# Kernel tuning notes

Hardware: AMD Instinct MI355X
Metric: run time of the kernel (lower is better)

The kernel has to match this reference:

```python
import jax, jax.numpy as jnp
import numpy as np

N_USERS = 100000
N_ITEMS = 200000
N_NODES = N_USERS + N_ITEMS
LATENT_DIM = 64
N_LAYERS = 3
NNZ = 6400000


def setup_inputs() -> dict:
    key = jax.random.key(0)
    k1, k2, k3, k4, k5 = jax.random.split(key, 5)
    user_emb = 0.1 * jax.random.normal(k1, (N_USERS, LATENT_DIM), dtype=jnp.float32)
    item_emb = 0.1 * jax.random.normal(k2, (N_ITEMS, LATENT_DIM), dtype=jnp.float32)
    rows = jax.random.randint(k3, (NNZ,), 0, N_NODES, dtype=jnp.int32)
    cols = jax.random.randint(k4, (NNZ,), 0, N_NODES, dtype=jnp.int32)
    # normalized-adjacency-like positive values
    vals = jax.random.uniform(k5, (NNZ,), dtype=jnp.float32) * 0.05
    return {"user_emb": user_emb, "item_emb": item_emb,
            "rows": rows, "cols": cols, "vals": vals}


def _spmm(rows, cols, vals, x):
    # y[r] += vals[e] * x[cols[e]]  for each edge e with rows[e]==r
    gathered = vals[:, None] * x[cols]          # [nnz, D]
    return jax.ops.segment_sum(gathered, rows, num_segments=N_NODES)


def reference(user_emb, item_emb, rows, cols, vals):
    # LightGCN.computer(): multi-hop propagation + layer mean pooling
    all_emb = jnp.concatenate([user_emb, item_emb], axis=0)   # [N, D]
    acc = all_emb
    for _ in range(N_LAYERS):
        all_emb = _spmm(rows, cols, vals, all_emb)
        acc = acc + all_emb
    light_out = acc / (N_LAYERS + 1)
    users = light_out[:N_USERS]
    items = light_out[N_USERS:]
    return users, items
```

## Files before the change

kernel.cpp:

```cpp
#include <hip/hip_runtime.h>
#include <hip/hip_bf16.h>

#define N_USERS 100000
#define N_ITEMS 200000
#define N_NODES 300000
#define DIM 64

#define TOT_ELEMS ((size_t)N_NODES * DIM)
#define TOT_F4    (TOT_ELEMS / 4)
#define USER_F4   (((size_t)N_USERS * DIM) / 4)

#define BROWS 512
#define NBUCKET ((N_NODES + BROWS - 1) / BROWS)
#define EPT 32
#define EDGES_PER_BLOCK (EPT * 256)

__device__ __forceinline__ float bf2f(unsigned short u) {
    return __uint_as_float((unsigned int)u << 16);
}
__device__ __forceinline__ unsigned short f2bf(float f) {
    __hip_bfloat16 h = __float2bfloat16(f);
    return *reinterpret_cast<unsigned short*>(&h);
}

__global__ void init_kernel(const float4* __restrict__ user,
                            const float4* __restrict__ item,
                            ushort4* __restrict__ xh) {
    size_t i = (size_t)blockIdx.x * blockDim.x + threadIdx.x;
    if (i >= TOT_F4) return;
    float4 v = (i < USER_F4) ? user[i] : item[i - USER_F4];
    ushort4 h;
    h.x = f2bf(v.x); h.y = f2bf(v.y); h.z = f2bf(v.z); h.w = f2bf(v.w);
    xh[i] = h;
}

__global__ void zero_buckets_kernel(int* __restrict__ bucket_count) {
    int i = blockIdx.x * blockDim.x + threadIdx.x;
    if (i < NBUCKET) bucket_count[i] = 0;
}

__global__ void bucket_hist_kernel(const int* __restrict__ rows,
                                   int* __restrict__ bucket_count, int nnz) {
    __shared__ int h[NBUCKET];
    int t = threadIdx.x;
    size_t base = (size_t)blockIdx.x * EDGES_PER_BLOCK;
    for (int i = t; i < NBUCKET; i += 256) h[i] = 0;
    __syncthreads();
    #pragma unroll 4
    for (int k = 0; k < EPT; ++k) {
        size_t e = base + (size_t)k * 256 + t;
        if (e < (size_t)nnz) atomicAdd(&h[rows[e] >> 9], 1);
    }
    __syncthreads();
    for (int i = t; i < NBUCKET; i += 256) {
        int c = h[i];
        if (c) atomicAdd(&bucket_count[i], c);
    }
}

__global__ void bucket_scan_kernel(const int* __restrict__ bucket_count,
                                   int* __restrict__ bucket_base,
                                   int* __restrict__ bucket_cursor, int nnz) {
    __shared__ int s[1024];
    int t = threadIdx.x;
    int orig = (t < NBUCKET) ? bucket_count[t] : 0;
    s[t] = orig;
    __syncthreads();
    for (int off = 1; off < 1024; off <<= 1) {
        int v = (t >= off) ? s[t - off] : 0;
        __syncthreads();
        s[t] += v;
        __syncthreads();
    }
    if (t < NBUCKET) {
        int excl = s[t] - orig;
        bucket_base[t]   = excl;
        bucket_cursor[t] = excl;
    }
    if (t == 0) bucket_base[NBUCKET] = nnz;
}

__global__ void binA_kernel(const int* __restrict__ rows,
                            const int* __restrict__ cols,
                            const float* __restrict__ vals,
                            int* __restrict__ bucket_cursor,
                            int2* __restrict__ binned,
                            int nnz) {
    __shared__ int h[NBUCKET];
    int t = threadIdx.x;
    size_t base = (size_t)blockIdx.x * EDGES_PER_BLOCK;
    for (int i = t; i < NBUCKET; i += 256) h[i] = 0;
    __syncthreads();
    #pragma unroll 4
    for (int k = 0; k < EPT; ++k) {
        size_t e = base + (size_t)k * 256 + t;
        if (e < (size_t)nnz) atomicAdd(&h[rows[e] >> 9], 1);
    }
    __syncthreads();
    for (int i = t; i < NBUCKET; i += 256) {
        int c = h[i];
        h[i] = (c > 0) ? atomicAdd(&bucket_cursor[i], c) : 0;
    }
    __syncthreads();
    #pragma unroll 4
    for (int k = 0; k < EPT; ++k) {
        size_t e = base + (size_t)k * 256 + t;
        if (e < (size_t)nnz) {
            int r = rows[e];
            int pos = atomicAdd(&h[r >> 9], 1);
            binned[pos] = make_int2(((r & (BROWS - 1)) << 19) | cols[e],
                                    __float_as_int(vals[e]));
        }
    }
}

__global__ void binB_kernel(const int* __restrict__ bucket_base,
                            const int2* __restrict__ binned,
                            int2* __restrict__ sorted,
                            int* __restrict__ row_ptr,
                            int nnz) {
    __shared__ int cnt[BROWS];
    __shared__ int cur[BROWS];
    __shared__ int s[256];
    int b = blockIdx.x, t = threadIdx.x;
    int beg = bucket_base[b];
    int end = bucket_base[b + 1];
    int row0 = b * BROWS;
    for (int i = t; i < BROWS; i += 256) cnt[i] = 0;
    __syncthreads();
    for (int idx = beg + t; idx < end; idx += 256) {
        int lr = ((unsigned)binned[idx].x) >> 19;
        atomicAdd(&cnt[lr], 1);
    }
    __syncthreads();
    int c0 = cnt[2 * t], c1 = cnt[2 * t + 1];
    int local = c0 + c1;
    s[t] = local;
    __syncthreads();
    for (int off = 1; off < 256; off <<= 1) {
        int v = (t >= off) ? s[t - off] : 0;
        __syncthreads();
        s[t] += v;
        __syncthreads();
    }
    int excl = beg + s[t] - local;
    int r0 = row0 + 2 * t;
    if (r0 < N_NODES)     row_ptr[r0]     = excl;
    if (r0 + 1 < N_NODES) row_ptr[r0 + 1] = excl + c0;
    cur[2 * t]     = excl;
    cur[2 * t + 1] = excl + c0;
    __syncthreads();
    for (int idx = beg + t; idx < end; idx += 256) {
        int2 e = binned[idx];
        int lr  = ((unsigned)e.x) >> 19;
        int col = e.x & 0x7FFFF;
        int pos = atomicAdd(&cur[lr], 1);
        sorted[pos] = make_int2(col, e.y);
    }
    if (b == 0 && t == 0) row_ptr[N_NODES] = nnz;
}

__device__ __forceinline__ float row_accum(int beg, int end, int d,
                                           const int2* __restrict__ sorted,
                                           const unsigned short* __restrict__ srch) {
    float acc = 0.f;
    for (int base = beg; base < end; base += 64) {
        int rem = end - base;
        int cnt = rem > 64 ? 64 : rem;
        int c_l = 0;
        int v_i = 0;
        if (base + d < end) {
            int2 e = sorted[base + d];
            c_l = e.x;
            v_i = e.y;
        }
        int j = 0;
        for (; j + 8 <= cnt; j += 8) {
            int c0 = __builtin_amdgcn_readlane(c_l, j + 0);
            int c1 = __builtin_amdgcn_readlane(c_l, j + 1);
            int c2 = __builtin_amdgcn_readlane(c_l, j + 2);
            int c3 = __builtin_amdgcn_readlane(c_l, j + 3);
            int c4 = __builtin_amdgcn_readlane(c_l, j + 4);
            int c5 = __builtin_amdgcn_readlane(c_l, j + 5);
            int c6 = __builtin_amdgcn_readlane(c_l, j + 6);
            int c7 = __builtin_amdgcn_readlane(c_l, j + 7);
            float s0 = bf2f(srch[(size_t)c0 * DIM + d]);
            float s1 = bf2f(srch[(size_t)c1 * DIM + d]);
            float s2 = bf2f(srch[(size_t)c2 * DIM + d]);
            float s3 = bf2f(srch[(size_t)c3 * DIM + d]);
            float s4 = bf2f(srch[(size_t)c4 * DIM + d]);
            float s5 = bf2f(srch[(size_t)c5 * DIM + d]);
            float s6 = bf2f(srch[(size_t)c6 * DIM + d]);
            float s7 = bf2f(srch[(size_t)c7 * DIM + d]);
            float v0 = __uint_as_float(__builtin_amdgcn_readlane(v_i, j + 0));
            float v1 = __uint_as_float(__builtin_amdgcn_readlane(v_i, j + 1));
            float v2 = __uint_as_float(__builtin_amdgcn_readlane(v_i, j + 2));
            float v3 = __uint_as_float(__builtin_amdgcn_readlane(v_i, j + 3));
            float v4 = __uint_as_float(__builtin_amdgcn_readlane(v_i, j + 4));
            float v5 = __uint_as_float(__builtin_amdgcn_readlane(v_i, j + 5));
            float v6 = __uint_as_float(__builtin_amdgcn_readlane(v_i, j + 6));
            float v7 = __uint_as_float(__builtin_amdgcn_readlane(v_i, j + 7));
            acc += v0 * s0; acc += v1 * s1; acc += v2 * s2; acc += v3 * s3;
            acc += v4 * s4; acc += v5 * s5; acc += v6 * s6; acc += v7 * s7;
        }
        for (; j + 4 <= cnt; j += 4) {
            int c0 = __builtin_amdgcn_readlane(c_l, j + 0);
            int c1 = __builtin_amdgcn_readlane(c_l, j + 1);
            int c2 = __builtin_amdgcn_readlane(c_l, j + 2);
            int c3 = __builtin_amdgcn_readlane(c_l, j + 3);
            float s0 = bf2f(srch[(size_t)c0 * DIM + d]);
            float s1 = bf2f(srch[(size_t)c1 * DIM + d]);
            float s2 = bf2f(srch[(size_t)c2 * DIM + d]);
            float s3 = bf2f(srch[(size_t)c3 * DIM + d]);
            float v0 = __uint_as_float(__builtin_amdgcn_readlane(v_i, j + 0));
            float v1 = __uint_as_float(__builtin_amdgcn_readlane(v_i, j + 1));
            float v2 = __uint_as_float(__builtin_amdgcn_readlane(v_i, j + 2));
            float v3 = __uint_as_float(__builtin_amdgcn_readlane(v_i, j + 3));
            acc += v0 * s0; acc += v1 * s1; acc += v2 * s2; acc += v3 * s3;
        }
        for (; j < cnt; ++j) {
            int c = __builtin_amdgcn_readlane(c_l, j);
            float v = __uint_as_float(__builtin_amdgcn_readlane(v_i, j));
            acc += v * bf2f(srch[(size_t)c * DIM + d]);
        }
    }
    return acc;
}

__global__ void spmm_row_kernel(const int* __restrict__ row_ptr,
                                const int2* __restrict__ sorted,
                                const unsigned short* __restrict__ srch,
                                unsigned short* __restrict__ dsth) {
    int t = blockIdx.x * blockDim.x + threadIdx.x;
    int r = t >> 6;
    int d = t & 63;
    if (r >= N_NODES) return;
    float acc = row_accum(row_ptr[r], row_ptr[r + 1], d, sorted, srch);
    dsth[(size_t)r * DIM + d] = f2bf(acc);
}

__global__ void spmm_final_kernel(const int* __restrict__ row_ptr,
                                  const int2* __restrict__ sorted,
                                  const unsigned short* __restrict__ y2h,
                                  const unsigned short* __restrict__ y1h,
                                  const float* __restrict__ user,
                                  const float* __restrict__ item,
                                  float* __restrict__ out) {
    int t = blockIdx.x * blockDim.x + threadIdx.x;
    int r = t >> 6;
    int d = t & 63;
    if (r >= N_NODES) return;
    float acc = row_accum(row_ptr[r], row_ptr[r + 1], d, sorted, y2h);
    size_t idx = (size_t)r * DIM + d;
    float base = (r < N_USERS) ? user[idx]
                               : item[idx - (size_t)N_USERS * DIM];
    out[idx] = 0.25f * (base + bf2f(y1h[idx]) + bf2f(y2h[idx]) + acc);
}

extern "C" void kernel_launch(void* const* d_in, const int* in_sizes, int n_in,
                              void* d_out, int out_size, void* d_ws, size_t ws_size,
                              hipStream_t stream) {
    const float* user = (const float*)d_in[0];
    const float* item = (const float*)d_in[1];
    const int*   rows = (const int*)d_in[2];
    const int*   cols = (const int*)d_in[3];
    const float* vals = (const float*)d_in[4];
    int nnz = in_sizes[2];

    float* out = (float*)d_out;

    char* p = (char*)d_ws;
    unsigned short* xh  = (unsigned short*)p; p += TOT_ELEMS * 2;
    unsigned short* y1h = (unsigned short*)p; p += TOT_ELEMS * 2;
    unsigned short* y2h = (unsigned short*)p; p += TOT_ELEMS * 2;
    int2* binned = (int2*)p; p += (size_t)nnz * sizeof(int2);
    int2* sorted = (int2*)p; p += (size_t)nnz * sizeof(int2);
    int* row_ptr       = (int*)p; p += (size_t)(N_NODES + 1) * 4;
    int* bucket_count  = (int*)p; p += (size_t)NBUCKET * 4;
    int* bucket_base   = (int*)p; p += (size_t)(NBUCKET + 1) * 4;
    int* bucket_cursor = (int*)p; p += (size_t)NBUCKET * 4;

    const int BLK = 256;
    int grid_elem = (int)((TOT_F4 + BLK - 1) / BLK);
    int grid_binA = (nnz + EDGES_PER_BLOCK - 1) / EDGES_PER_BLOCK;
    int grid_rows = (N_NODES * 64 + BLK - 1) / BLK;

    init_kernel<<<grid_elem, BLK, 0, stream>>>(
        (const float4*)user, (const float4*)item, (ushort4*)xh);

    zero_buckets_kernel<<<(NBUCKET + BLK - 1) / BLK, BLK, 0, stream>>>(bucket_count);
    bucket_hist_kernel<<<grid_binA, BLK, 0, stream>>>(rows, bucket_count, nnz);
    bucket_scan_kernel<<<1, 1024, 0, stream>>>(bucket_count, bucket_base, bucket_cursor, nnz);

    binA_kernel<<<grid_binA, BLK, 0, stream>>>(rows, cols, vals, bucket_cursor, binned, nnz);
    binB_kernel<<<NBUCKET, BLK, 0, stream>>>(bucket_base, binned, sorted, row_ptr, nnz);

    spmm_row_kernel<<<grid_rows, BLK, 0, stream>>>(row_ptr, sorted, xh,  y1h);
    spmm_row_kernel<<<grid_rows, BLK, 0, stream>>>(row_ptr, sorted, y1h, y2h);
    spmm_final_kernel<<<grid_rows, BLK, 0, stream>>>(row_ptr, sorted, y2h, y1h,
                                                     user, item, out);
}
```

Measured before the change: 916.0 us.

## Split wavefront into two edge halves gathering packed bf16 pairs per lane

The row SpMM kernel now has each 32-lane half of a wavefront handle alternate edges. Each lane loads a 32-bit pair of bf16 features and keeps two accumulators, and the halves are combined with a cross-half shuffle at the end. Edge indices are broadcast with ds_bpermute instead of scalar readlane, so each half gets a different edge. The goal is to halve the number of gather load instructions per edge and widen each access. Nontemporal loads and stores are also added to the streaming reads in init, binning and the final combine. The cost is an extra shuffle reduction and LDS-permute traffic per edge.

After: 887.8 us. -3.1%, faster.

```diff
diff --git a/kernel.cpp b/kernel.cpp
--- a/kernel.cpp
+++ b/kernel.cpp
@@ -15,6 +15,8 @@
 #define EPT 32
 #define EDGES_PER_BLOCK (EPT * 256)
 
+typedef float f4_native __attribute__((ext_vector_type(4)));
+
 __device__ __forceinline__ float bf2f(unsigned short u) {
     return __uint_as_float((unsigned int)u << 16);
 }
@@ -22,13 +24,21 @@
     __hip_bfloat16 h = __float2bfloat16(f);
     return *reinterpret_cast<unsigned short*>(&h);
 }
-
-__global__ void init_kernel(const float4* __restrict__ user,
-                            const float4* __restrict__ item,
+__device__ __forceinline__ float lo_bf(unsigned int u) {
+    return __uint_as_float(u << 16);
+}
+__device__ __forceinline__ float hi_bf(unsigned int u) {
+    return __uint_as_float(u & 0xFFFF0000u);
+}
+
+__global__ void init_kernel(const float* __restrict__ user,
+                            const float* __restrict__ item,
                             ushort4* __restrict__ xh) {
     size_t i = (size_t)blockIdx.x * blockDim.x + threadIdx.x;
     if (i >= TOT_F4) return;
-    float4 v = (i < USER_F4) ? user[i] : item[i - USER_F4];
+    f4_native v = (i < USER_F4)
+        ? __builtin_nontemporal_load((const f4_native*)user + i)
+        : __builtin_nontemporal_load((const f4_native*)item + (i - USER_F4));
     ushort4 h;
     h.x = f2bf(v.x); h.y = f2bf(v.y); h.z = f2bf(v.z); h.w = f2bf(v.w);
     xh[i] = h;
@@ -108,8 +118,10 @@
         if (e < (size_t)nnz) {
             int r = rows[e];
             int pos = atomicAdd(&h[r >> 9], 1);
-            binned[pos] = make_int2(((r & (BROWS - 1)) << 19) | cols[e],
-                                    __float_as_int(vals[e]));
+            int c   = __builtin_nontemporal_load(cols + e);
+            float v = __builtin_nontemporal_load(vals + e);
+            binned[pos] = make_int2(((r & (BROWS - 1)) << 19) | c,
+                                    __float_as_int(v));
         }
     }
 }
@@ -160,71 +172,92 @@
     if (b == 0 && t == 0) row_ptr[N_NODES] = nnz;
 }
 
-__device__ __forceinline__ float row_accum(int beg, int end, int d,
+__device__ __forceinline__ void row_accum2(int beg, int end, int l,
                                            const int2* __restrict__ sorted,
-                                           const unsigned short* __restrict__ srch) {
-    float acc = 0.f;
+                                           const unsigned short* __restrict__ srch,
+                                           float& r0, float& r1) {
+    const int h4 = (l >> 5) << 2;
+    const unsigned int q = (unsigned)(l & 31);
+    const unsigned int* __restrict__ srcd = (const unsigned int*)srch;
+    float acc0 = 0.f, acc1 = 0.f;
+
     for (int base = beg; base < end; base += 64) {
         int rem = end - base;
         int cnt = rem > 64 ? 64 : rem;
-        int c_l = 0;
-        int v_i = 0;
-        if (base + d < end) {
-            int2 e = sorted[base + d];
-            c_l = e.x;
-            v_i = e.y;
-        }
-        int j = 0;
-        for (; j + 8 <= cnt; j += 8) {
-            int c0 = __builtin_amdgcn_readlane(c_l, j + 0);
-            int c1 = __builtin_amdgcn_readlane(c_l, j + 1);
-            int c2 = __builtin_amdgcn_readlane(c_l, j + 2);
-            int c3 = __builtin_amdgcn_readlane(c_l, j + 3);
-            int c4 = __builtin_amdgcn_readlane(c_l, j + 4);
-            int c5 = __builtin_amdgcn_readlane(c_l, j + 5);
-            int c6 = __builtin_amdgcn_readlane(c_l, j + 6);
-            int c7 = __builtin_amdgcn_readlane(c_l, j + 7);
-            float s0 = bf2f(srch[(size_t)c0 * DIM + d]);
-            float s1 = bf2f(srch[(size_t)c1 * DIM + d]);
-            float s2 = bf2f(srch[(size_t)c2 * DIM + d]);
-            float s3 = bf2f(srch[(size_t)c3 * DIM + d]);
-            float s4 = bf2f(srch[(size_t)c4 * DIM + d]);
-            float s5 = bf2f(srch[(size_t)c5 * DIM + d]);
-            float s6 = bf2f(srch[(size_t)c6 * DIM + d]);
-            float s7 = bf2f(srch[(size_t)c7 * DIM + d]);
-            float v0 = __uint_as_float(__builtin_amdgcn_readlane(v_i, j + 0));
-            float v1 = __uint_as_float(__builtin_amdgcn_readlane(v_i, j + 1));
-            float v2 = __uint_as_float(__builtin_amdgcn_readlane(v_i, j + 2));
-            float v3 = __uint_as_float(__builtin_amdgcn_readlane(v_i, j + 3));
-            float v4 = __uint_as_float(__builtin_amdgcn_readlane(v_i, j + 4));
-            float v5 = __uint_as_float(__builtin_amdgcn_readlane(v_i, j + 5));
-            float v6 = __uint_as_float(__builtin_amdgcn_readlane(v_i, j + 6));
-            float v7 = __uint_as_float(__builtin_amdgcn_readlane(v_i, j + 7));
-            acc += v0 * s0; acc += v1 * s1; acc += v2 * s2; acc += v3 * s3;
-            acc += v4 * s4; acc += v5 * s5; acc += v6 * s6; acc += v7 * s7;
-        }
-        for (; j + 4 <= cnt; j += 4) {
-            int c0 = __builtin_amdgcn_readlane(c_l, j + 0);
-            int c1 = __builtin_amdgcn_readlane(c_l, j + 1);
-            int c2 = __builtin_amdgcn_readlane(c_l, j + 2);
-            int c3 = __builtin_amdgcn_readlane(c_l, j + 3);
-            float s0 = bf2f(srch[(size_t)c0 * DIM + d]);
-            float s1 = bf2f(srch[(size_t)c1 * DIM + d]);
-            float s2 = bf2f(srch[(size_t)c2 * DIM + d]);
-            float s3 = bf2f(srch[(size_t)c3 * DIM + d]);
-            float v0 = __uint_as_float(__builtin_amdgcn_readlane(v_i, j + 0));
-            float v1 = __uint_as_float(__builtin_amdgcn_readlane(v_i, j + 1));
-            float v2 = __uint_as_float(__builtin_amdgcn_readlane(v_i, j + 2));
-            float v3 = __uint_as_float(__builtin_amdgcn_readlane(v_i, j + 3));
-            acc += v0 * s0; acc += v1 * s1; acc += v2 * s2; acc += v3 * s3;
-        }
-        for (; j < cnt; ++j) {
-            int c = __builtin_amdgcn_readlane(c_l, j);
-            float v = __uint_as_float(__builtin_amdgcn_readlane(v_i, j));
-            acc += v * bf2f(srch[(size_t)c * DIM + d]);
-        }
-    }
-    return acc;
+        int c_l = 0, v_l = 0;
+        if (base + l < end) {
+            unsigned long long e = __builtin_nontemporal_load(
+                (const unsigned long long*)sorted + base + l);
+            c_l = (int)(unsigned int)(e & 0xFFFFFFFFull);
+            v_l = (int)(unsigned int)(e >> 32);
+        }
+        int npairs = (cnt + 1) >> 1;
+        int p = 0;
+        for (; p + 8 <= npairs; p += 8) {
+            int i0 = h4 + (p << 3);
+            int c0 = __builtin_amdgcn_ds_bpermute(i0 +  0, c_l);
+            int c1 = __builtin_amdgcn_ds_bpermute(i0 +  8, c_l);
+            int c2 = __builtin_amdgcn_ds_bpermute(i0 + 16, c_l);
+            int c3 = __builtin_amdgcn_ds_bpermute(i0 + 24, c_l);
+            int c4 = __builtin_amdgcn_ds_bpermute(i0 + 32, c_l);
+            int c5 = __builtin_amdgcn_ds_bpermute(i0 + 40, c_l);
+            int c6 = __builtin_amdgcn_ds_bpermute(i0 + 48, c_l);
+            int c7 = __builtin_amdgcn_ds_bpermute(i0 + 56, c_l);
+            unsigned int u0 = srcd[((unsigned int)c0 << 5) | q];
+            unsigned int u1 = srcd[((unsigned int)c1 << 5) | q];
+            unsigned int u2 = srcd[((unsigned int)c2 << 5) | q];
+            unsigned int u3 = srcd[((unsigned int)c3 << 5) | q];
+            unsigned int u4 = srcd[((unsigned int)c4 << 5) | q];
+            unsigned int u5 = srcd[((unsigned int)c5 << 5) | q];
+            unsigned int u6 = srcd[((unsigned int)c6 << 5) | q];
+            unsigned int u7 = srcd[((unsigned int)c7 << 5) | q];
+            float v0 = __int_as_float(__builtin_amdgcn_ds_bpermute(i0 +  0, v_l));
+            float v1 = __int_as_float(__builtin_amdgcn_ds_bpermute(i0 +  8, v_l));
+            float v2 = __int_as_float(__builtin_amdgcn_ds_bpermute(i0 + 16, v_l));
+            float v3 = __int_as_float(__builtin_amdgcn_ds_bpermute(i0 + 24, v_l));
+            float v4 = __int_as_float(__builtin_amdgcn_ds_bpermute(i0 + 32, v_l));
+            float v5 = __int_as_float(__builtin_amdgcn_ds_bpermute(i0 + 40, v_l));
+            float v6 = __int_as_float(__builtin_amdgcn_ds_bpermute(i0 + 48, v_l));
+            float v7 = __int_as_float(__builtin_amdgcn_ds_bpermute(i0 + 56, v_l));
+            acc0 = fmaf(v0, lo_bf(u0), acc0); acc1 = fmaf(v0, hi_bf(u0), acc1);
+            acc0 = fmaf(v1, lo_bf(u1), acc0); acc1 = fmaf(v1, hi_bf(u1), acc1);
+            acc0 = fmaf(v2, lo_bf(u2), acc0); acc1 = fmaf(v2, hi_bf(u2), acc1);
+            acc0 = fmaf(v3, lo_bf(u3), acc0); acc1 = fmaf(v3, hi_bf(u3), acc1);
+            acc0 = fmaf(v4, lo_bf(u4), acc0); acc1 = fmaf(v4, hi_bf(u4), acc1);
+            acc0 = fmaf(v5, lo_bf(u5), acc0); acc1 = fmaf(v5, hi_bf(u5), acc1);
+            acc0 = fmaf(v6, lo_bf(u6), acc0); acc1 = fmaf(v6, hi_bf(u6), acc1);
+            acc0 = fmaf(v7, lo_bf(u7), acc0); acc1 = fmaf(v7, hi_bf(u7), acc1);
+        }
+        for (; p + 4 <= npairs; p += 4) {
+            int i0 = h4 + (p << 3);
+            int c0 = __builtin_amdgcn_ds_bpermute(i0 +  0, c_l);
+            int c1 = __builtin_amdgcn_ds_bpermute(i0 +  8, c_l);
+            int c2 = __builtin_amdgcn_ds_bpermute(i0 + 16, c_l);
+            int c3 = __builtin_amdgcn_ds_bpermute(i0 + 24, c_l);
+            unsigned int u0 = srcd[((unsigned int)c0 << 5) | q];
+            unsigned int u1 = srcd[((unsigned int)c1 << 5) | q];
+            unsigned int u2 = srcd[((unsigned int)c2 << 5) | q];
+            unsigned int u3 = srcd[((unsigned int)c3 << 5) | q];
+            float v0 = __int_as_float(__builtin_amdgcn_ds_bpermute(i0 +  0, v_l));
+            float v1 = __int_as_float(__builtin_amdgcn_ds_bpermute(i0 +  8, v_l));
+            float v2 = __int_as_float(__builtin_amdgcn_ds_bpermute(i0 + 16, v_l));
+            float v3 = __int_as_float(__builtin_amdgcn_ds_bpermute(i0 + 24, v_l));
+            acc0 = fmaf(v0, lo_bf(u0), acc0); acc1 = fmaf(v0, hi_bf(u0), acc1);
+            acc0 = fmaf(v1, lo_bf(u1), acc0); acc1 = fmaf(v1, hi_bf(u1), acc1);
+            acc0 = fmaf(v2, lo_bf(u2), acc0); acc1 = fmaf(v2, hi_bf(u2), acc1);
+            acc0 = fmaf(v3, lo_bf(u3), acc0); acc1 = fmaf(v3, hi_bf(u3), acc1);
+        }
+        for (; p < npairs; ++p) {
+            int i0 = h4 + (p << 3);
+            int c0 = __builtin_amdgcn_ds_bpermute(i0, c_l);
+            unsigned int u0 = srcd[((unsigned int)c0 << 5) | q];
+            float v0 = __int_as_float(__builtin_amdgcn_ds_bpermute(i0, v_l));
+            acc0 = fmaf(v0, lo_bf(u0), acc0);
+            acc1 = fmaf(v0, hi_bf(u0), acc1);
+        }
+    }
+    r0 = acc0 + __shfl_xor(acc0, 32);
+    r1 = acc1 + __shfl_xor(acc1, 32);
 }
 
 __global__ void spmm_row_kernel(const int* __restrict__ row_ptr,
@@ -233,10 +266,14 @@
                                 unsigned short* __restrict__ dsth) {
     int t = blockIdx.x * blockDim.x + threadIdx.x;
     int r = t >> 6;
-    int d = t & 63;
+    int l = t & 63;
     if (r >= N_NODES) return;
-    float acc = row_accum(row_ptr[r], row_ptr[r + 1], d, sorted, srch);
-    dsth[(size_t)r * DIM + d] = f2bf(acc);
+    float r0, r1;
+    row_accum2(row_ptr[r], row_ptr[r + 1], l, sorted, srch, r0, r1);
+    if (l < 32) {
+        unsigned int pack = (unsigned int)f2bf(r0) | ((unsigned int)f2bf(r1) << 16);
+        ((unsigned int*)dsth)[(size_t)r * 32 + l] = pack;
+    }
 }
 
 __global__ void spmm_final_kernel(const int* __restrict__ row_ptr,
@@ -248,13 +285,23 @@
                                   float* __restrict__ out) {
     int t = blockIdx.x * blockDim.x + threadIdx.x;
     int r = t >> 6;
-    int d = t & 63;
+    int l = t & 63;
     if (r >= N_NODES) return;
-    float acc = row_accum(row_ptr[r], row_ptr[r + 1], d, sorted, y2h);
-    size_t idx = (size_t)r * DIM + d;
-    float base = (r < N_USERS) ? user[idx]
-                               : item[idx - (size_t)N_USERS * DIM];
-    out[idx] = 0.25f * (base + bf2f(y1h[idx]) + bf2f(y2h[idx]) + acc);
+    float r0, r1;
+    row_accum2(row_ptr[r], row_ptr[r + 1], l, sorted, y2h, r0, r1);
+    if (l < 32) {
+        size_t didx = (size_t)r * 32 + l;
+        unsigned int y1d = __builtin_nontemporal_load((const unsigned int*)y1h + didx);
+        unsigned int y2d = __builtin_nontemporal_load((const unsigned int*)y2h + didx);
+        const float* bp = (r < N_USERS) ? (user + 2 * didx)
+                                        : (item + 2 * (didx - (size_t)N_USERS * 32));
+        float b0 = __builtin_nontemporal_load(bp + 0);
+        float b1 = __builtin_nontemporal_load(bp + 1);
+        float o0 = 0.25f * (b0 + lo_bf(y1d) + lo_bf(y2d) + r0);
+        float o1 = 0.25f * (b1 + hi_bf(y1d) + hi_bf(y2d) + r1);
+        __builtin_nontemporal_store(o0, out + 2 * didx + 0);
+        __builtin_nontemporal_store(o1, out + 2 * didx + 1);
+    }
 }
 
 extern "C" void kernel_launch(void* const* d_in, const int* in_sizes, int n_in,
@@ -285,8 +332,7 @@
     int grid_binA = (nnz + EDGES_PER_BLOCK - 1) / EDGES_PER_BLOCK;
     int grid_rows = (N_NODES * 64 + BLK - 1) / BLK;
 
-    init_kernel<<<grid_elem, BLK, 0, stream>>>(
-        (const float4*)user, (const float4*)item, (ushort4*)xh);
+    init_kernel<<<grid_elem, BLK, 0, stream>>>(user, item, (ushort4*)xh);
 
     zero_buckets_kernel<<<(NBUCKET + BLK - 1) / BLK, BLK, 0, stream>>>(bucket_count);
     bucket_hist_kernel<<<grid_binA, BLK, 0, stream>>>(rows, bucket_count, nnz);
```
